# Kernel optimization log

Hardware: AMD Instinct MI355X
Metric: run time of the kernel (lower is better)

Reference implementation:

```python
import jax, jax.numpy as jnp
import numpy as np

# Module hyperparameters (from init_kwargs)
B, C, E, T = 8, 128, 128, 128          # batch, in_channels, embedding(freq), time
O, G, KW, KS = 256, 4, 9, 1            # out_channels, groups, kernel_width, kernel_stride
D = C // G                              # kernel depth per group = 32
N = O // G                              # filters per group = 64
AH, AS = 2, 2                           # activate_height, activate_stride
NEG_SLOPE = 0.01                        # nn.LeakyReLU default


def setup_inputs() -> dict:
    key = jax.random.key(0)
    kx, kw = jax.random.split(key)
    x = jax.random.normal(kx, (B, C, E, T), dtype=jnp.float32)
    # xavier_uniform over (O, D, E, KW): fan_in = D*E*KW, fan_out = O*E*KW
    fan_in, fan_out = D * E * KW, O * E * KW
    limit = float(np.sqrt(6.0 / (fan_in + fan_out)))
    weight = jax.random.uniform(kw, (O, D, E, KW), dtype=jnp.float32,
                                minval=-limit, maxval=limit)
    return {"x": x, "weight": weight}


def reference(x, weight):
    b, c, e, t = x.shape
    # --- symmetric-ish zero pad along time so unfold yields exactly t windows ---
    pad = (t - 1) * KS - t + KW
    xp = jnp.pad(x, ((0, 0), (0, 0), (0, 0), (pad // 2, (pad + 1) // 2)))
    # --- unfold: windows of size KW at stride KS -> (b, c, e, t, KW) ---
    idx = jnp.arange(t)[:, None] * KS + jnp.arange(KW)[None, :]  # (t, KW)
    xu = xp[..., idx]                                            # (b, c, e, t, KW)
    # --- grouped linear-conv: instead of materializing (b,t,g,n,d,e,KW), contract d,KW ---
    xu = xu.reshape(b, G, D, e, t, KW)                 # (b, g, d, e, t, w)
    wr = weight.reshape(G, N, D, e, KW)                # (g, n, d, e, w)
    # z[b,g,n,e,t] = sum_{d,w} xu * wr  (the all-ones conv sums over d and full width w)
    z = jnp.einsum('bgdetw,gndew->bgnet', xu, wr).reshape(b, O, e, t)
    # --- all-ones conv height pooling: kernel AH, stride AS over e (valid) ---
    f_out = (e - AH) // AS + 1
    cs = jnp.cumsum(z, axis=2)
    cs = jnp.concatenate([jnp.zeros_like(cs[:, :, :1]), cs], axis=2)  # prefix sums
    pos = jnp.arange(f_out) * AS
    pooled = cs[:, :, pos + AH, :] - cs[:, :, pos, :]   # (b, O, f_out, t)
    # --- LeakyReLU ---
    y = jnp.where(pooled >= 0, pooled, NEG_SLOPE * pooled)
    return y  # (b, o, f_out, t), matching 'b o f t'
```

## Files before the change

### kernel.cpp

```cpp
#include <hip/hip_runtime.h>
#include <cstddef>

typedef __attribute__((ext_vector_type(8))) short short8v;
typedef __attribute__((ext_vector_type(4))) short short4v;
typedef __attribute__((ext_vector_type(4))) float f32x4;

__device__ __forceinline__ unsigned short f2bf(float f) {
    unsigned u = __float_as_uint(f);
    u = (u + 0x7FFFu + ((u >> 16) & 1u)) >> 16;
    return (unsigned short)u;
}

__global__ __launch_bounds__(256) void prep_w(const float* __restrict__ w,
                                              unsigned short* __restrict__ wb)
{
    const int g  = blockIdx.x >> 6;
    const int f  = blockIdx.x & 63;
    const int e0 = 2 * f;
    const int tid = threadIdx.x;
    __shared__ unsigned short ls[64 * 580];

    #pragma unroll 4
    for (int i = 0; i < 72; ++i) {
        int fl  = tid + i * 256;
        int od  = fl / 9;
        int f2i = fl - od * 9;
        int o_l = od >> 5;
        int d   = od & 31;
        const float2 v = *reinterpret_cast<const float2*>(
            &w[(size_t)((g * 64 + o_l) * 32 + d) * 1152 + e0 * 9 + f2i * 2]);
        ushort2 hh; hh.x = f2bf(v.x); hh.y = f2bf(v.y);
        *reinterpret_cast<ushort2*>(&ls[o_l * 580 + d * 18 + f2i * 2]) = hh;
    }
    __syncthreads();

    unsigned short* wo = wb + (size_t)(g * 64 + f) * 36864;
    #pragma unroll 2
    for (int i = 0; i < 18; ++i) {
        int oc   = tid + i * 256;
        int ks   = oc >> 8;
        int nt   = (oc >> 6) & 3;
        int lane = oc & 63;
        int li = lane & 15, hi = lane >> 4;
        int e  = (ks >= 9) ? 1 : 0;
        int w9 = ks - 9 * e;
        int o_l = nt * 16 + li;
        short8v vv;
        #pragma unroll
        for (int j = 0; j < 8; ++j)
            vv[j] = (short)ls[o_l * 580 + (hi * 8 + j) * 18 + e * 9 + w9];
        int half = (w9 < 5) ? 0 : 1;
        int w9l  = w9 - 5 * half;
        size_t off = (size_t)e * 18432 + half * 10240 + (w9l * 4 + nt) * 512 + lane * 8;
        *reinterpret_cast<short8v*>(&wo[off]) = vv;
    }
}

__global__ __launch_bounds__(256, 3) void lconv_mfma(const float* __restrict__ x,
                                                     const unsigned short* __restrict__ wb,
                                                     float* __restrict__ out)
{
    int bid = blockIdx.x;
    int lid = (bid & 7) * 128 + (bid >> 3);
    const int bp = lid & 3;
    const int f  = (lid >> 2) & 63;
    const int g  = lid >> 8;
    const int e0 = 2 * f;

    const int tid  = threadIdx.x;
    const int lane = tid & 63;
    const int wv   = tid >> 6;
    const int bl   = wv & 1;
    const int th   = wv >> 1;
    const int li   = lane & 15;
    const int hi   = lane >> 4;
    const int t    = tid & 127;
    const int z    = tid >> 7;

    __shared__ __align__(16) unsigned short xs[2 * 136 * 40];
    __shared__ __align__(16) unsigned short As[10240];

    if (tid < 128) {
        int blz = tid >> 6;
        int r   = (tid >> 3) & 7;
        int dq  = tid & 7;
        int tp  = (r < 4) ? r : (128 + r);
        short4v zz = {0, 0, 0, 0};
        *reinterpret_cast<short4v*>(&xs[(blz * 136 + tp) * 40 + dq * 4]) = zz;
    }

    const unsigned short* wA = wb + (size_t)(g * 64 + f) * 36864;

    float   xr[32];
    short8v ar[5];

    f32x4 acc[4][4];
    #pragma unroll
    for (int nt = 0; nt < 4; ++nt)
        #pragma unroll
        for (int tt = 0; tt < 4; ++tt)
            acc[nt][tt] = (f32x4){0.f, 0.f, 0.f, 0.f};

    auto issueX = [&](int ec) {
        const int e  = e0 + ec;
        const int b0 = bp * 2 + z;
        const float* xp0 = &x[((size_t)(b0 * 128 + g * 32) * 128 + e) * 128 + t];
        #pragma unroll
        for (int dq = 0; dq < 8; ++dq) {
            const float* xp = xp0 + (size_t)dq * 4 * 16384;
            xr[dq * 4 + 0] = xp[0];
            xr[dq * 4 + 1] = xp[16384];
            xr[dq * 4 + 2] = xp[32768];
            xr[dq * 4 + 3] = xp[49152];
        }
    };
    auto lwriteX = [&]() {
        #pragma unroll
        for (int dq = 0; dq < 8; ++dq) {
            short4v hq;
            hq[0] = (short)f2bf(xr[dq * 4 + 0]);
            hq[1] = (short)f2bf(xr[dq * 4 + 1]);
            hq[2] = (short)f2bf(xr[dq * 4 + 2]);
            hq[3] = (short)f2bf(xr[dq * 4 + 3]);
            *reinterpret_cast<short4v*>(&xs[(z * 136 + t + 4) * 40 + dq * 4]) = hq;
        }
    };
    auto issueA = [&](int ec, int h) {
        const short8v* src = reinterpret_cast<const short8v*>(
            wA + (size_t)ec * 18432 + h * 10240);
        const int cnt = h ? 4 : 5;
        #pragma unroll
        for (int i = 0; i < 5; ++i)
            if (i < cnt) ar[i] = src[tid + i * 256];
    };
    auto lwriteA = [&](int h) {
        short8v* dst = reinterpret_cast<short8v*>(As);
        const int cnt = h ? 4 : 5;
        #pragma unroll
        for (int i = 0; i < 5; ++i)
            if (i < cnt) dst[tid + i * 256] = ar[i];
    };
    auto compute = [&](int h) {
        const int cnt = h ? 4 : 5;
        const int wb9 = h ? 5 : 0;
        #pragma unroll
        for (int w9l = 0; w9l < 5; ++w9l) {
            if (w9l >= cnt) break;
            short8v Af[4], Bf[4];
            #pragma unroll
            for (int nt = 0; nt < 4; ++nt)
                Af[nt] = *reinterpret_cast<const short8v*>(
                    &As[(w9l * 4 + nt) * 512 + lane * 8]);
            #pragma unroll
            for (int tt = 0; tt < 4; ++tt) {
                int tp = th * 64 + tt * 16 + li + wb9 + w9l;
                Bf[tt] = *reinterpret_cast<const short8v*>(
                    &xs[(bl * 136 + tp) * 40 + hi * 8]);
            }
            __builtin_amdgcn_s_setprio(1);
            #pragma unroll
            for (int nt = 0; nt < 4; ++nt)
                #pragma unroll
                for (int tt = 0; tt < 4; ++tt)
                    acc[nt][tt] = __builtin_amdgcn_mfma_f32_16x16x32_bf16(
                        Af[nt], Bf[tt], acc[nt][tt], 0, 0, 0);
            __builtin_amdgcn_s_setprio(0);
        }
    };

    issueX(0); issueA(0, 0);
    lwriteX(); lwriteA(0);
    __syncthreads();

    issueA(0, 1);
    compute(0);
    __syncthreads();
    lwriteA(1);
    __syncthreads();

    issueX(1);
    compute(1);
    __syncthreads();
    lwriteX();
    issueA(1, 0);
    lwriteA(0);
    __syncthreads();

    issueA(1, 1);
    compute(0);
    __syncthreads();
    lwriteA(1);
    __syncthreads();

    compute(1);

    const int b = bp * 2 + bl;
    #pragma unroll
    for (int nt = 0; nt < 4; ++nt) {
        #pragma unroll
        for (int tt = 0; tt < 4; ++tt) {
            #pragma unroll
            for (int j = 0; j < 4; ++j) {
                float v = acc[nt][tt][j];
                v = (v >= 0.f) ? v : 0.01f * v;
                int n  = nt * 16 + hi * 4 + j;
                int tc = th * 64 + tt * 16 + li;
                out[(((size_t)(b * 256 + g * 64 + n)) * 64 + f) * 128 + tc] = v;
            }
        }
    }
}

extern "C" void kernel_launch(void* const* d_in, const int* in_sizes, int n_in,
                              void* d_out, int out_size, void* d_ws, size_t ws_size,
                              hipStream_t stream)
{
    const float* x = (const float*)d_in[0];
    const float* w = (const float*)d_in[1];
    float* out = (float*)d_out;
    unsigned short* wb = (unsigned short*)d_ws;

    hipLaunchKernelGGL(prep_w, dim3(256), dim3(256), 0, stream, w, wb);
    hipLaunchKernelGGL(lconv_mfma, dim3(1024), dim3(256), 0, stream, x, wb, out);
}
```

Baseline: 61.64 us.

## Load weight fragments directly from global memory and drop LDS staging

The weight tiles are no longer staged through LDS. Each wave now reads its MFMA A-fragments straight from global memory in a simple linear layout that prep_w writes by index. The hand-written software pipeline that overlapped the next x/weight loads with compute is replaced by a plain loop over the two e rows, and the x loads are split into two passes to cut register use. Occupancy is raised to 4 blocks per SM. This removes LDS traffic and barriers for weights, but weight loads now sit on the critical path with less overlap, and all four waves per block issue redundant global reads.

```diff
diff --git a/kernel.cpp b/kernel.cpp
--- a/kernel.cpp
+++ b/kernel.cpp
@@ -49,14 +49,11 @@
         #pragma unroll
         for (int j = 0; j < 8; ++j)
             vv[j] = (short)ls[o_l * 580 + (hi * 8 + j) * 18 + e * 9 + w9];
-        int half = (w9 < 5) ? 0 : 1;
-        int w9l  = w9 - 5 * half;
-        size_t off = (size_t)e * 18432 + half * 10240 + (w9l * 4 + nt) * 512 + lane * 8;
-        *reinterpret_cast<short8v*>(&wo[off]) = vv;
+        *reinterpret_cast<short8v*>(&wo[(size_t)oc * 8]) = vv;
     }
 }
 
-__global__ __launch_bounds__(256, 3) void lconv_mfma(const float* __restrict__ x,
+__global__ __launch_bounds__(256, 4) void lconv_mfma(const float* __restrict__ x,
                                                      const unsigned short* __restrict__ wb,
                                                      float* __restrict__ out)
 {
@@ -78,7 +75,6 @@
     const int z    = tid >> 7;
 
     __shared__ __align__(16) unsigned short xs[2 * 136 * 40];
-    __shared__ __align__(16) unsigned short As[10240];
 
     if (tid < 128) {
         int blz = tid >> 6;
@@ -91,9 +87,6 @@
 
     const unsigned short* wA = wb + (size_t)(g * 64 + f) * 36864;
 
-    float   xr[32];
-    short8v ar[5];
-
     f32x4 acc[4][4];
     #pragma unroll
     for (int nt = 0; nt < 4; ++nt)
@@ -101,59 +94,45 @@
         for (int tt = 0; tt < 4; ++tt)
             acc[nt][tt] = (f32x4){0.f, 0.f, 0.f, 0.f};
 
-    auto issueX = [&](int ec) {
-        const int e  = e0 + ec;
-        const int b0 = bp * 2 + z;
-        const float* xp0 = &x[((size_t)(b0 * 128 + g * 32) * 128 + e) * 128 + t];
+    for (int ec = 0; ec < 2; ++ec) {
+        if (ec) __syncthreads();
+
         #pragma unroll
-        for (int dq = 0; dq < 8; ++dq) {
-            const float* xp = xp0 + (size_t)dq * 4 * 16384;
-            xr[dq * 4 + 0] = xp[0];
-            xr[dq * 4 + 1] = xp[16384];
-            xr[dq * 4 + 2] = xp[32768];
-            xr[dq * 4 + 3] = xp[49152];
+        for (int pass = 0; pass < 2; ++pass) {
+            float xr[16];
+            #pragma unroll
+            for (int dqi = 0; dqi < 4; ++dqi) {
+                const int dq = pass * 4 + dqi;
+                const float* xp = &x[(size_t)(((bp * 2 + z) * 128 + g * 32 + dq * 4) * 128
+                                              + (e0 + ec)) * 128 + t];
+                xr[dqi * 4 + 0] = xp[0];
+                xr[dqi * 4 + 1] = xp[16384];
+                xr[dqi * 4 + 2] = xp[32768];
+                xr[dqi * 4 + 3] = xp[49152];
+            }
+            #pragma unroll
+            for (int dqi = 0; dqi < 4; ++dqi) {
+                const int dq = pass * 4 + dqi;
+                short4v hq;
+                hq[0] = (short)f2bf(xr[dqi * 4 + 0]);
+                hq[1] = (short)f2bf(xr[dqi * 4 + 1]);
+                hq[2] = (short)f2bf(xr[dqi * 4 + 2]);
+                hq[3] = (short)f2bf(xr[dqi * 4 + 3]);
+                *reinterpret_cast<short4v*>(&xs[(z * 136 + t + 4) * 40 + dq * 4]) = hq;
+            }
         }
-    };
-    auto lwriteX = [&]() {
+        __syncthreads();
+
         #pragma unroll
-        for (int dq = 0; dq < 8; ++dq) {
-            short4v hq;
-            hq[0] = (short)f2bf(xr[dq * 4 + 0]);
-            hq[1] = (short)f2bf(xr[dq * 4 + 1]);
-            hq[2] = (short)f2bf(xr[dq * 4 + 2]);
-            hq[3] = (short)f2bf(xr[dq * 4 + 3]);
-            *reinterpret_cast<short4v*>(&xs[(z * 136 + t + 4) * 40 + dq * 4]) = hq;
-        }
-    };
-    auto issueA = [&](int ec, int h) {
-        const short8v* src = reinterpret_cast<const short8v*>(
-            wA + (size_t)ec * 18432 + h * 10240);
-        const int cnt = h ? 4 : 5;
-        #pragma unroll
-        for (int i = 0; i < 5; ++i)
-            if (i < cnt) ar[i] = src[tid + i * 256];
-    };
-    auto lwriteA = [&](int h) {
-        short8v* dst = reinterpret_cast<short8v*>(As);
-        const int cnt = h ? 4 : 5;
-        #pragma unroll
-        for (int i = 0; i < 5; ++i)
-            if (i < cnt) dst[tid + i * 256] = ar[i];
-    };
-    auto compute = [&](int h) {
-        const int cnt = h ? 4 : 5;
-        const int wb9 = h ? 5 : 0;
-        #pragma unroll
-        for (int w9l = 0; w9l < 5; ++w9l) {
-            if (w9l >= cnt) break;
+        for (int w9 = 0; w9 < 9; ++w9) {
             short8v Af[4], Bf[4];
             #pragma unroll
             for (int nt = 0; nt < 4; ++nt)
                 Af[nt] = *reinterpret_cast<const short8v*>(
-                    &As[(w9l * 4 + nt) * 512 + lane * 8]);
+                    &wA[(size_t)((ec * 9 + w9) * 4 + nt) * 512 + lane * 8]);
             #pragma unroll
             for (int tt = 0; tt < 4; ++tt) {
-                int tp = th * 64 + tt * 16 + li + wb9 + w9l;
+                int tp = th * 64 + tt * 16 + li + w9;
                 Bf[tt] = *reinterpret_cast<const short8v*>(
                     &xs[(bl * 136 + tp) * 40 + hi * 8]);
             }
@@ -166,33 +145,7 @@
                         Af[nt], Bf[tt], acc[nt][tt], 0, 0, 0);
             __builtin_amdgcn_s_setprio(0);
         }
-    };
-
-    issueX(0); issueA(0, 0);
-    lwriteX(); lwriteA(0);
-    __syncthreads();
-
-    issueA(0, 1);
-    compute(0);
-    __syncthreads();
-    lwriteA(1);
-    __syncthreads();
-
-    issueX(1);
-    compute(1);
-    __syncthreads();
-    lwriteX();
-    issueA(1, 0);
-    lwriteA(0);
-    __syncthreads();
-
-    issueA(1, 1);
-    compute(0);
-    __syncthreads();
-    lwriteA(1);
-    __syncthreads();
-
-    compute(1);
+    }
 
     const int b = bp * 2 + bl;
     #pragma unroll
```

New measurement: 57.04 us. -7.5%, faster.
